# Optimization experiments

Hardware: AMD Instinct MI355X
Metric: run time of the kernel (lower is better)

Reference implementation:

```python
import math
import jax, jax.numpy as jnp
import numpy as np

NUM_TOKENS = 8192
MODEL_DIM = 1024
NUM_EXPERTS = 64
CAPACITY_FACTOR = 1.0
MIN_CAPACITY = 8
SHIFT_PRIORITY = 0.5
LOAD_BALANCE_W = 0.01


def setup_inputs() -> dict:
    key = jax.random.key(0)
    k1, k2 = jax.random.split(key)
    x = jax.random.normal(k1, (NUM_TOKENS, MODEL_DIM), dtype=jnp.float32)
    # torch.nn.Linear(model_dim, num_experts, bias=False).weight -> [E, D]
    wg_weight = jax.random.normal(k2, (NUM_EXPERTS, MODEL_DIM), dtype=jnp.float32) * 0.02
    return {"x": x, "wg_weight": wg_weight}


def reference(x, wg_weight):
    S = x.shape[0]
    E = wg_weight.shape[0]
    # gate projection (fp32, as in DeepSpeed gating)
    logits = jnp.einsum('sd,ed->se', x, wg_weight)  # [S, E]
    gates = jax.nn.softmax(logits, axis=1)
    original_gates = gates

    # _capacity: ceil(S/E * capacity_factor), clamped to min_capacity (static)
    capacity = max(int(math.ceil(S / E * CAPACITY_FACTOR)), MIN_CAPACITY)

    indices1_s = jnp.argmax(gates, axis=1)                      # [S]
    mask1 = jax.nn.one_hot(indices1_s, E, dtype=jnp.int32)      # [S, E]
    exp_counts = jnp.sum(mask1, axis=0)                         # [E]

    # AuxLoss: GShard load-balance loss, zloss/entropy weights are 0
    me = jnp.mean(gates, axis=0)
    ce = jnp.mean(mask1.astype(gates.dtype), axis=0)
    l_aux = jnp.sum(me * ce) * E * LOAD_BALANCE_W

    # shifted-priority routing: sort tokens by -max_gate, roll, positional cumsum
    importance_scores = -jnp.max(gates, axis=1)                 # [S]
    sort_indices = jnp.argsort(importance_scores)               # [S]
    shift_num = int(S * SHIFT_PRIORITY)                         # static
    sort_indices = jnp.roll(sort_indices, shift_num)
    recover_indices = jnp.argsort(sort_indices)
    sorted_mask1 = mask1[sort_indices]                          # [S, E]
    sorted_cumsum1 = (jnp.cumsum(sorted_mask1, axis=0) - 1) * sorted_mask1
    locations1 = sorted_cumsum1[recover_indices]                # [S, E]

    # capacity dropping
    mask1 = mask1 * (locations1 < capacity).astype(jnp.int32)
    locations1_s = jnp.sum(locations1 * mask1, axis=1)          # [S]

    gates_masked = original_gates * mask1.astype(gates.dtype)   # [S, E]
    locations1_sc = jax.nn.one_hot(locations1_s, capacity, dtype=gates.dtype)  # [S, C]
    combine_weights = jnp.einsum('se,sc->sec', gates_masked, locations1_sc)    # [S, E, C]
    dispatch_mask = combine_weights.astype(bool)

    unrouted_token_rate = 1.0 - jnp.mean(jnp.any(dispatch_mask, axis=(-1, -2)).astype(jnp.float32))
    return l_aux, combine_weights, dispatch_mask, exp_counts, unrouted_token_rate
```

## Files before the change

### kernel.cpp

```cpp
#include <hip/hip_runtime.h>
#include <stdint.h>

#define S_TOK   8192
#define MODEL_D 1024
#define N_EXP   64
#define CAP     128
#define SHIFT   4096
#define SLAB    (N_EXP * CAP)
#define CDSIZE  ((size_t)S_TOK * SLAB)
#define OUT_FILL4 33554448

#define GEMM_BLOCKS 512
#define TPB         16


#define OFF_EXPERT   0
#define OFF_GATE     32768
#define OFF_KEY      65536
#define OFF_KEY2     98304
#define OFF_MEPART   131072
#define OFF_HIST     262144
#define OFF_WGT      393216

__device__ __forceinline__ unsigned f2key(float f) {
    unsigned b = __float_as_uint(f);
    return (b & 0x80000000u) ? ~b : (b | 0x80000000u);
}

__global__ __launch_bounds__(256) void k0_repack(const float* __restrict__ wg,
                                                 float* __restrict__ wgT4) {
    int id0 = blockIdx.x * 256 + threadIdx.x;
#pragma unroll
    for (int i = 0; i < 4; ++i) {
        int id = id0 + i * 16384;
        int e = id >> 10;
        int d = id & 1023;
        wgT4[((d >> 2) * 64 + e) * 4 + (d & 3)] = wg[id];
    }
}

__global__ __launch_bounds__(256) void k1_fill_gemm(
    const float* __restrict__ x, const float* __restrict__ wgT4,
    float* __restrict__ out,
    int* __restrict__ expert_id, float* __restrict__ gate1,
    unsigned* __restrict__ keys, float* __restrict__ me_part,
    int* __restrict__ hist_part)
{
    const int b = blockIdx.x;
    if (b >= GEMM_BLOCKS) {
        const float4 z = make_float4(0.f, 0.f, 0.f, 0.f);
        float4* out4 = (float4*)out;
        size_t i = (size_t)(b - GEMM_BLOCKS) * 256 + threadIdx.x;
        for (; i < OUT_FILL4; i += (size_t)8192 * 256) out4[i] = z;
        return;
    }

    __shared__ float xs[TPB][256];
    __shared__ float lg[TPB][65];
    __shared__ float mrow[TPB], zrow[TPB];
    __shared__ int   exrow[TPB];
    __shared__ int   hist[64];
    __shared__ float mep[4][64];

    const int tid  = threadIdx.x;
    const int lane = tid & 63;
    const int wv   = tid >> 6;
    const int tok0 = b * TPB;

    const float4* xg  = (const float4*)x;
    const float4* wg4 = (const float4*)wgT4;

    float acc[4] = {0.f, 0.f, 0.f, 0.f};

    for (int chunk = 0; chunk < 4; ++chunk) {
        __syncthreads();
#pragma unroll
        for (int i = 0; i < 4; ++i) {
            int linear = tid + 256 * i;
            int t  = linear >> 6;
            int c4 = linear & 63;
            ((float4*)xs)[t * 64 + c4] = xg[(size_t)(tok0 + t) * 256 + chunk * 64 + c4];
        }
        __syncthreads();

#pragma unroll 4
        for (int dd = 0; dd < 256; dd += 4) {
            int d = chunk * 256 + dd;
            float4 w = wg4[(d >> 2) * 64 + lane];
#pragma unroll
            for (int t = 0; t < 4; ++t) {
                float4 xv = *(const float4*)&xs[wv * 4 + t][dd];
                acc[t] = fmaf(xv.x, w.x, acc[t]);
                acc[t] = fmaf(xv.y, w.y, acc[t]);
                acc[t] = fmaf(xv.z, w.z, acc[t]);
                acc[t] = fmaf(xv.w, w.w, acc[t]);
            }
        }
    }
#pragma unroll
    for (int t = 0; t < 4; ++t) lg[wv * 4 + t][lane] = acc[t];
    __syncthreads();

    if (tid < 64) hist[tid] = 0;
    if (tid < TPB) {
        const int t = tid;
        float m = lg[t][0]; int am = 0;
        for (int e = 1; e < 64; ++e) {
            float v = lg[t][e];
            if (v > m) { m = v; am = e; }
        }
        float z = 0.f;
        for (int e = 0; e < 64; ++e) z += expf(lg[t][e] - m);
        float rz = 1.0f / z;
        mrow[t] = m; zrow[t] = rz; exrow[t] = am;
        int sG = tok0 + t;
        expert_id[sG] = am;
        gate1[sG] = rz;
        keys[sG] = f2key(-rz);
    }
    __syncthreads();

    if (tid < TPB) atomicAdd(&hist[exrow[tid]], 1);
    {
        const int e = tid & 63, tg = tid >> 6;
        float p = 0.f;
        for (int t = tg; t < TPB; t += 4) p += expf(lg[t][e] - mrow[t]) * zrow[t];
        mep[tg][e] = p;
    }
    __syncthreads();

    if (tid < 64) {
        me_part[b * 64 + tid] = mep[0][tid] + mep[1][tid] + mep[2][tid] + mep[3][tid];
        hist_part[b * 64 + tid] = hist[tid];
    }
}

__global__ __launch_bounds__(256) void k2_rank_scalars(
    const unsigned* __restrict__ keys, const int* __restrict__ expert_id,
    const float* __restrict__ me_part, const int* __restrict__ hist_part,
    unsigned* __restrict__ key2, float* __restrict__ out)
{
    const int tid = threadIdx.x;
    if (blockIdx.x == 256) {
        __shared__ float msum[4][64];
        __shared__ int   hsum[4][64];
        __shared__ float contrib[64];
        __shared__ int   keep[64];
        const int e = tid & 63, qt = tid >> 6;
        float ms = 0.f; int hs = 0;
        for (int p = qt * 128; p < qt * 128 + 128; ++p) {
            ms += me_part[p * 64 + e];
            hs += hist_part[p * 64 + e];
        }
        msum[qt][e] = ms; hsum[qt][e] = hs;
        __syncthreads();
        if (tid < 64) {
            float m = msum[0][tid] + msum[1][tid] + msum[2][tid] + msum[3][tid];
            int   h = hsum[0][tid] + hsum[1][tid] + hsum[2][tid] + hsum[3][tid];
            out[1 + 2 * CDSIZE + tid] = (float)h;
            contrib[tid] = (m * (1.0f / S_TOK)) * ((float)h * (1.0f / S_TOK));
            keep[tid] = (h < CAP) ? h : CAP;
        }
        __syncthreads();
        if (tid == 0) {
            float sum = 0.f; int kept = 0;
            for (int i = 0; i < 64; ++i) { sum += contrib[i]; kept += keep[i]; }
            out[0] = sum * (float)N_EXP * 0.01f;
            out[1 + 2 * CDSIZE + 64] = (float)(S_TOK - kept) * (1.0f / S_TOK);
        }
        return;
    }

    __shared__ uint4 k4[2048];
    const uint4* kg = (const uint4*)keys;
    for (int i = tid; i < 2048; i += 256) k4[i] = kg[i];
    __syncthreads();

    const int sl = tid >> 3, part = tid & 7;
    const int sG = blockIdx.x * 32 + sl;
    const unsigned myk = ((const unsigned*)k4)[sG];
    int cnt = 0;
    const int qbase = part * 256;
    for (int q = 0; q < 256; ++q) {
        int qq = (q + part) & 255;
        uint4 v = k4[qbase + qq];
        int j = (qbase + qq) * 4;
        cnt += (v.x < myk) || (v.x == myk && (j + 0) < sG);
        cnt += (v.y < myk) || (v.y == myk && (j + 1) < sG);
        cnt += (v.z < myk) || (v.z == myk && (j + 2) < sG);
        cnt += (v.w < myk) || (v.w == myk && (j + 3) < sG);
    }
    cnt += __shfl_down(cnt, 4);
    cnt += __shfl_down(cnt, 2);
    cnt += __shfl_down(cnt, 1);
    if (part == 0) {
        int pos = (cnt + SHIFT) & (S_TOK - 1);
        key2[sG] = ((unsigned)expert_id[sG] << 13) | (unsigned)pos;
    }
}

__global__ __launch_bounds__(256) void k3_loc_scatter(const unsigned* __restrict__ key2,
                                                      const float* __restrict__ gate1,
                                                      float* __restrict__ out)
{
    __shared__ uint4 k4[2048];
    const int tid = threadIdx.x;
    const uint4* kg = (const uint4*)key2;
    for (int i = tid; i < 2048; i += 256) k4[i] = kg[i];
    __syncthreads();

    const int sl = tid >> 3, part = tid & 7;
    const int sG = blockIdx.x * 32 + sl;
    const unsigned myk = ((const unsigned*)k4)[sG];
    const unsigned lo = myk & ~8191u;
    int cnt = 0;
    const int qbase = part * 256;
    for (int q = 0; q < 256; ++q) {
        int qq = (q + part) & 255;
        uint4 v = k4[qbase + qq];
        cnt += (v.x >= lo) && (v.x < myk);
        cnt += (v.y >= lo) && (v.y < myk);
        cnt += (v.z >= lo) && (v.z < myk);
        cnt += (v.w >= lo) && (v.w < myk);
    }
    cnt += __shfl_down(cnt, 4);
    cnt += __shfl_down(cnt, 2);
    cnt += __shfl_down(cnt, 1);
    if (part == 0 && cnt < CAP) {
        unsigned e = myk >> 13;
        size_t idx = 1 + (size_t)sG * SLAB + (size_t)e * CAP + (unsigned)cnt;
        out[idx] = gate1[sG];
        out[idx + CDSIZE] = 1.0f;
    }
}

extern "C" void kernel_launch(void* const* d_in, const int* in_sizes, int n_in,
                              void* d_out, int out_size, void* d_ws, size_t ws_size,
                              hipStream_t stream) {
    (void)in_sizes; (void)n_in; (void)out_size; (void)ws_size;
    const float* x  = (const float*)d_in[0];
    const float* wg = (const float*)d_in[1];
    float* out = (float*)d_out;
    char* ws = (char*)d_ws;

    int*      expert_id = (int*)(ws + OFF_EXPERT);
    float*    gate1     = (float*)(ws + OFF_GATE);
    unsigned* keys      = (unsigned*)(ws + OFF_KEY);
    unsigned* key2      = (unsigned*)(ws + OFF_KEY2);
    float*    me_part   = (float*)(ws + OFF_MEPART);
    int*      hist_part = (int*)(ws + OFF_HIST);
    float*    wgT4      = (float*)(ws + OFF_WGT);

    hipLaunchKernelGGL(k0_repack,       dim3(64),                dim3(256), 0, stream, wg, wgT4);
    hipLaunchKernelGGL(k1_fill_gemm,    dim3(GEMM_BLOCKS + 8192), dim3(256), 0, stream,
                       x, wgT4, out, expert_id, gate1, keys, me_part, hist_part);
    hipLaunchKernelGGL(k2_rank_scalars, dim3(257),               dim3(256), 0, stream,
                       keys, expert_id, me_part, hist_part, key2, out);
    hipLaunchKernelGGL(k3_loc_scatter,  dim3(256),               dim3(256), 0, stream,
                       key2, gate1, out);
}
```

Baseline: 714.3 us.

## Fuse all stages into one cooperative kernel with grid-wide syncs

Replaces the four separate launches (repack, fill+GEMM, rank, scatter) with a single cooperative persistent kernel of 512 blocks that uses grid.sync between stages and a shared-memory union. It aims to remove launch gaps and inter-kernel overhead. The large output zero-fill now runs before the GEMM behind a grid barrier, not overlapped with it, and uses far fewer blocks. If the cooperative launch fails, it falls back to the old multi-kernel path.

Result: slower. 851.5 us (+19.2%).

```diff
diff --git a/kernel.cpp b/kernel.cpp
--- a/kernel.cpp
+++ b/kernel.cpp
@@ -1,5 +1,8 @@
 #include <hip/hip_runtime.h>
+#include <hip/hip_cooperative_groups.h>
 #include <stdint.h>
+
+namespace cg = cooperative_groups;
 
 #define S_TOK   8192
 #define MODEL_D 1024
@@ -10,6 +13,7 @@
 #define CDSIZE  ((size_t)S_TOK * SLAB)
 #define OUT_FILL4 33554448
 
+#define GRID_BLOCKS 512
 #define GEMM_BLOCKS 512
 #define TPB         16
 
@@ -27,9 +31,11 @@
     return (b & 0x80000000u) ? ~b : (b | 0x80000000u);
 }
 
-__global__ __launch_bounds__(256) void k0_repack(const float* __restrict__ wg,
-                                                 float* __restrict__ wgT4) {
-    int id0 = blockIdx.x * 256 + threadIdx.x;
+
+__device__ __forceinline__ void repack_block(const float* __restrict__ wg,
+                                             float* __restrict__ wgT4,
+                                             int b, int tid) {
+    int id0 = b * 256 + tid;
 #pragma unroll
     for (int i = 0; i < 4; ++i) {
         int id = id0 + i * 16384;
@@ -37,6 +43,210 @@
         int d = id & 1023;
         wgT4[((d >> 2) * 64 + e) * 4 + (d & 3)] = wg[id];
     }
+}
+
+
+__global__ __launch_bounds__(256, 2) void k_all(
+    const float* __restrict__ x, const float* __restrict__ wg,
+    float* __restrict__ out, float* __restrict__ wgT4,
+    int* __restrict__ expert_id, float* __restrict__ gate1,
+    unsigned* __restrict__ keys, unsigned* __restrict__ key2,
+    float* __restrict__ me_part, int* __restrict__ hist_part)
+{
+    __shared__ union {
+        struct {
+            float xs[TPB][256];
+            float lg[TPB][65];
+            float mrow[TPB], zrow[TPB];
+            int   exrow[TPB];
+            int   hist[64];
+            float mep[4][64];
+        } g;
+        uint4 k4[2048];
+        struct {
+            float msum[4][64];
+            int   hsum[4][64];
+            float contrib[64];
+            int   keep[64];
+        } s;
+    } sh;
+
+    cg::grid_group grid = cg::this_grid();
+    const int b   = blockIdx.x;
+    const int tid = threadIdx.x;
+
+    if (b < 64) repack_block(wg, wgT4, b, tid);
+    {
+        const float4 z = make_float4(0.f, 0.f, 0.f, 0.f);
+        float4* out4 = (float4*)out;
+        for (size_t i = (size_t)b * 256 + tid; i < OUT_FILL4; i += (size_t)GRID_BLOCKS * 256)
+            out4[i] = z;
+    }
+    grid.sync();
+
+    {
+        const int lane = tid & 63;
+        const int wv   = tid >> 6;
+        const int tok0 = b * TPB;
+        const float4* xg  = (const float4*)x;
+        const float4* wg4 = (const float4*)wgT4;
+
+        float acc[4] = {0.f, 0.f, 0.f, 0.f};
+        for (int chunk = 0; chunk < 4; ++chunk) {
+            __syncthreads();
+#pragma unroll
+            for (int i = 0; i < 4; ++i) {
+                int linear = tid + 256 * i;
+                int t  = linear >> 6;
+                int c4 = linear & 63;
+                ((float4*)sh.g.xs)[t * 64 + c4] =
+                    xg[(size_t)(tok0 + t) * 256 + chunk * 64 + c4];
+            }
+            __syncthreads();
+#pragma unroll 4
+            for (int dd = 0; dd < 256; dd += 4) {
+                int d = chunk * 256 + dd;
+                float4 w = wg4[(d >> 2) * 64 + lane];
+#pragma unroll
+                for (int t = 0; t < 4; ++t) {
+                    float4 xv = *(const float4*)&sh.g.xs[wv * 4 + t][dd];
+                    acc[t] = fmaf(xv.x, w.x, acc[t]);
+                    acc[t] = fmaf(xv.y, w.y, acc[t]);
+                    acc[t] = fmaf(xv.z, w.z, acc[t]);
+                    acc[t] = fmaf(xv.w, w.w, acc[t]);
+                }
+            }
+        }
+#pragma unroll
+        for (int t = 0; t < 4; ++t) sh.g.lg[wv * 4 + t][lane] = acc[t];
+        __syncthreads();
+
+        if (tid < 64) sh.g.hist[tid] = 0;
+        if (tid < TPB) {
+            const int t = tid;
+            float m = sh.g.lg[t][0]; int am = 0;
+            for (int e = 1; e < 64; ++e) {
+                float v = sh.g.lg[t][e];
+                if (v > m) { m = v; am = e; }
+            }
+            float z = 0.f;
+            for (int e = 0; e < 64; ++e) z += expf(sh.g.lg[t][e] - m);
+            float rz = 1.0f / z;
+            sh.g.mrow[t] = m; sh.g.zrow[t] = rz; sh.g.exrow[t] = am;
+            int sG = tok0 + t;
+            expert_id[sG] = am;
+            gate1[sG] = rz;
+            keys[sG] = f2key(-rz);
+        }
+        __syncthreads();
+
+        if (tid < TPB) atomicAdd(&sh.g.hist[sh.g.exrow[tid]], 1);
+        {
+            const int e = tid & 63, tg = tid >> 6;
+            float p = 0.f;
+            for (int t = tg; t < TPB; t += 4)
+                p += expf(sh.g.lg[t][e] - sh.g.mrow[t]) * sh.g.zrow[t];
+            sh.g.mep[tg][e] = p;
+        }
+        __syncthreads();
+
+        if (tid < 64) {
+            me_part[b * 64 + tid] = sh.g.mep[0][tid] + sh.g.mep[1][tid]
+                                  + sh.g.mep[2][tid] + sh.g.mep[3][tid];
+            hist_part[b * 64 + tid] = sh.g.hist[tid];
+        }
+    }
+    grid.sync();
+
+    if (b < 256) {
+        const uint4* kg = (const uint4*)keys;
+        for (int i = tid; i < 2048; i += 256) sh.k4[i] = kg[i];
+        __syncthreads();
+
+        const int sl = tid >> 3, part = tid & 7;
+        const int sG = b * 32 + sl;
+        const unsigned myk = ((const unsigned*)sh.k4)[sG];
+        int cnt = 0;
+        const int qbase = part * 256;
+        for (int q = 0; q < 256; ++q) {
+            int qq = (q + part) & 255;
+            uint4 v = sh.k4[qbase + qq];
+            int j = (qbase + qq) * 4;
+            cnt += (v.x < myk) || (v.x == myk && (j + 0) < sG);
+            cnt += (v.y < myk) || (v.y == myk && (j + 1) < sG);
+            cnt += (v.z < myk) || (v.z == myk && (j + 2) < sG);
+            cnt += (v.w < myk) || (v.w == myk && (j + 3) < sG);
+        }
+        cnt += __shfl_down(cnt, 4);
+        cnt += __shfl_down(cnt, 2);
+        cnt += __shfl_down(cnt, 1);
+        if (part == 0) {
+            int pos = (cnt + SHIFT) & (S_TOK - 1);
+            key2[sG] = ((unsigned)expert_id[sG] << 13) | (unsigned)pos;
+        }
+    } else if (b == 256) {
+        const int e = tid & 63, qt = tid >> 6;
+        float ms = 0.f; int hs = 0;
+        for (int p = qt * 128; p < qt * 128 + 128; ++p) {
+            ms += me_part[p * 64 + e];
+            hs += hist_part[p * 64 + e];
+        }
+        sh.s.msum[qt][e] = ms; sh.s.hsum[qt][e] = hs;
+        __syncthreads();
+        if (tid < 64) {
+            float m = sh.s.msum[0][tid] + sh.s.msum[1][tid]
+                    + sh.s.msum[2][tid] + sh.s.msum[3][tid];
+            int   h = sh.s.hsum[0][tid] + sh.s.hsum[1][tid]
+                    + sh.s.hsum[2][tid] + sh.s.hsum[3][tid];
+            out[1 + 2 * CDSIZE + tid] = (float)h;
+            sh.s.contrib[tid] = (m * (1.0f / S_TOK)) * ((float)h * (1.0f / S_TOK));
+            sh.s.keep[tid] = (h < CAP) ? h : CAP;
+        }
+        __syncthreads();
+        if (tid == 0) {
+            float sum = 0.f; int kept = 0;
+            for (int i = 0; i < 64; ++i) { sum += sh.s.contrib[i]; kept += sh.s.keep[i]; }
+            out[0] = sum * (float)N_EXP * 0.01f;
+            out[1 + 2 * CDSIZE + 64] = (float)(S_TOK - kept) * (1.0f / S_TOK);
+        }
+    }
+    grid.sync();
+
+    if (b < 256) {
+        const uint4* kg = (const uint4*)key2;
+        for (int i = tid; i < 2048; i += 256) sh.k4[i] = kg[i];
+        __syncthreads();
+
+        const int sl = tid >> 3, part = tid & 7;
+        const int sG = b * 32 + sl;
+        const unsigned myk = ((const unsigned*)sh.k4)[sG];
+        const unsigned lo = myk & ~8191u;
+        int cnt = 0;
+        const int qbase = part * 256;
+        for (int q = 0; q < 256; ++q) {
+            int qq = (q + part) & 255;
+            uint4 v = sh.k4[qbase + qq];
+            cnt += (v.x >= lo) && (v.x < myk);
+            cnt += (v.y >= lo) && (v.y < myk);
+            cnt += (v.z >= lo) && (v.z < myk);
+            cnt += (v.w >= lo) && (v.w < myk);
+        }
+        cnt += __shfl_down(cnt, 4);
+        cnt += __shfl_down(cnt, 2);
+        cnt += __shfl_down(cnt, 1);
+        if (part == 0 && cnt < CAP) {
+            unsigned e = myk >> 13;
+            size_t idx = 1 + (size_t)sG * SLAB + (size_t)e * CAP + (unsigned)cnt;
+            out[idx] = gate1[sG];
+            out[idx + CDSIZE] = 1.0f;
+        }
+    }
+}
+
+
+__global__ __launch_bounds__(256) void k0_repack(const float* __restrict__ wg,
+                                                 float* __restrict__ wgT4) {
+    repack_block(wg, wgT4, blockIdx.x, threadIdx.x);
 }
 
 __global__ __launch_bounds__(256) void k1_fill_gemm(
@@ -71,7 +281,6 @@
     const float4* wg4 = (const float4*)wgT4;
 
     float acc[4] = {0.f, 0.f, 0.f, 0.f};
-
     for (int chunk = 0; chunk < 4; ++chunk) {
         __syncthreads();
 #pragma unroll
@@ -82,7 +291,6 @@
             ((float4*)xs)[t * 64 + c4] = xg[(size_t)(tok0 + t) * 256 + chunk * 64 + c4];
         }
         __syncthreads();
-
 #pragma unroll 4
         for (int dd = 0; dd < 256; dd += 4) {
             int d = chunk * 256 + dd;
@@ -243,19 +451,27 @@
     float* out = (float*)d_out;
     char* ws = (char*)d_ws;
 
+    float*    wgT4      = (float*)(ws + OFF_WGT);
     int*      expert_id = (int*)(ws + OFF_EXPERT);
     float*    gate1     = (float*)(ws + OFF_GATE);
     unsigned* keys      = (unsigned*)(ws + OFF_KEY);
     unsigned* key2      = (unsigned*)(ws + OFF_KEY2);
     float*    me_part   = (float*)(ws + OFF_MEPART);
     int*      hist_part = (int*)(ws + OFF_HIST);
-    float*    wgT4      = (float*)(ws + OFF_WGT);
-
-    hipLaunchKernelGGL(k0_repack,       dim3(64),                dim3(256), 0, stream, wg, wgT4);
-    hipLaunchKernelGGL(k1_fill_gemm,    dim3(GEMM_BLOCKS + 8192), dim3(256), 0, stream,
-                       x, wgT4, out, expert_id, gate1, keys, me_part, hist_part);
-    hipLaunchKernelGGL(k2_rank_scalars, dim3(257),               dim3(256), 0, stream,
-                       keys, expert_id, me_part, hist_part, key2, out);
-    hipLaunchKernelGGL(k3_loc_scatter,  dim3(256),               dim3(256), 0, stream,
-                       key2, gate1, out);
-}
+
+    void* args[] = { (void*)&x, (void*)&wg, (void*)&out, (void*)&wgT4,
+                     (void*)&expert_id, (void*)&gate1, (void*)&keys, (void*)&key2,
+                     (void*)&me_part, (void*)&hist_part };
+    hipError_t err = hipLaunchCooperativeKernel((const void*)k_all, dim3(GRID_BLOCKS),
+                                                dim3(256), args, 0, stream);
+    if (err != hipSuccess) {
+        (void)hipGetLastError();
+        hipLaunchKernelGGL(k0_repack,       dim3(64),                 dim3(256), 0, stream, wg, wgT4);
+        hipLaunchKernelGGL(k1_fill_gemm,    dim3(GEMM_BLOCKS + 8192), dim3(256), 0, stream,
+                           x, wgT4, out, expert_id, gate1, keys, me_part, hist_part);
+        hipLaunchKernelGGL(k2_rank_scalars, dim3(257),                dim3(256), 0, stream,
+                           keys, expert_id, me_part, hist_part, key2, out);
+        hipLaunchKernelGGL(k3_loc_scatter,  dim3(256),                dim3(256), 0, stream,
+                           key2, gate1, out);
+    }
+}
```
